# Optimization experiments

Hardware: AMD Instinct MI355X
Metric: run time of the kernel (lower is better)

Reference implementation:

```python
import jax, jax.numpy as jnp
import numpy as np

WS = (2, 7, 7)  # window size (T, H, W)
NUM_HEADS = 8


def _relative_position_index():
    t, h, w = WS
    coords = np.stack(np.meshgrid(np.arange(t), np.arange(h), np.arange(w), indexing='ij'))  # (3,t,h,w)
    flat = coords.reshape(3, -1)  # (3, N)
    rel = flat[:, :, None] - flat[:, None, :]  # (3, N, N)
    rel = rel.transpose(1, 2, 0).astype(np.int32)  # (N, N, 3)
    rel[..., 0] += t - 1
    rel[..., 1] += h - 1
    rel[..., 2] += w - 1
    rel[..., 0] *= (2 * h - 1) * (2 * w - 1)
    rel[..., 1] *= 2 * w - 1
    return rel.sum(-1)  # (N, N)


def setup_inputs() -> dict:
    key = jax.random.key(0)
    ks = jax.random.split(key, 7)
    B_, N, C = 2048, 98, 256
    nW = 512
    table_size = (2 * WS[0] - 1) * (2 * WS[1] - 1) * (2 * WS[2] - 1)  # 507
    return {
        'x': jax.random.normal(ks[0], (B_, N, C), jnp.float32),
        'mask': jax.random.normal(ks[1], (nW, N, N), jnp.float32),
        'qkv_w': jax.random.normal(ks[2], (3 * C, C), jnp.float32) * 0.02,
        'qkv_b': jax.random.normal(ks[3], (3 * C,), jnp.float32) * 0.02,
        'proj_w': jax.random.normal(ks[4], (C, C), jnp.float32) * 0.02,
        'proj_b': jax.random.normal(ks[5], (C,), jnp.float32) * 0.02,
        'bias_table': jax.random.normal(ks[6], (table_size, NUM_HEADS), jnp.float32) * 0.02,
        'rel_index': jnp.asarray(_relative_position_index()),
    }


def reference(x, mask, qkv_w, qkv_b, proj_w, proj_b, bias_table, rel_index):
    B_, N, C = x.shape
    H = NUM_HEADS
    hd = C // H
    scale = hd ** -0.5
    # QKV projection -> (3, B_, H, N, hd)
    qkv = (x @ qkv_w.T + qkv_b).reshape(B_, N, 3, H, hd).transpose(2, 0, 3, 1, 4)
    q, k, v = qkv[0], qkv[1], qkv[2]
    attn = jnp.einsum('bhnd,bhmd->bhnm', q * scale, k)  # (B_, H, N, N)
    # gathered relative-position bias -> (H, N, N)
    bias = bias_table[rel_index.reshape(-1)].reshape(N, N, H).transpose(2, 0, 1)
    attn = attn + bias[None]
    nW = mask.shape[0]
    attn = attn.reshape(B_ // nW, nW, H, N, N) + mask[None, :, None]
    attn = jax.nn.softmax(attn.reshape(B_, H, N, N), axis=-1)
    out = jnp.einsum('bhnm,bhmd->bhnd', attn, v)  # (B_, H, N, hd)
    out = out.transpose(0, 2, 1, 3).reshape(B_, N, C)
    return out @ proj_w.T + proj_b
```

## Files before the change

kernel.cpp:

```cpp
#include <hip/hip_runtime.h>
#include <hip/hip_bf16.h>

typedef __attribute__((ext_vector_type(8))) short short8;
typedef __attribute__((ext_vector_type(4))) float f32x4;

__device__ __forceinline__ unsigned short f2bf(float f) {
    __hip_bfloat16 h = __float2bfloat16(f);
    union { __hip_bfloat16 h; unsigned short u; } c; c.h = h; return c.u;
}

typedef __attribute__((address_space(1))) const unsigned int gas_u32;
typedef __attribute__((address_space(3))) unsigned int las_u32;

__device__ __forceinline__ void gload_lds16(const unsigned short* g, unsigned short* l) {
    __builtin_amdgcn_global_load_lds((gas_u32*)g, (las_u32*)l, 16, 0, 0);
}

__global__ void cvt_bf16_kernel(const float* __restrict__ src,
                                unsigned short* __restrict__ dst, long n8) {
    long stride = (long)gridDim.x * 256;
    for (long t = (long)blockIdx.x * 256 + threadIdx.x; t < n8; t += stride) {
        long i = t * 8;
        float4 f0 = *reinterpret_cast<const float4*>(src + i);
        float4 f1 = *reinterpret_cast<const float4*>(src + i + 4);
        uint4 u;
        u.x = ((unsigned)f2bf(f0.y) << 16) | f2bf(f0.x);
        u.y = ((unsigned)f2bf(f0.w) << 16) | f2bf(f0.z);
        u.z = ((unsigned)f2bf(f1.y) << 16) | f2bf(f1.x);
        u.w = ((unsigned)f2bf(f1.w) << 16) | f2bf(f1.z);
        *reinterpret_cast<uint4*>(dst + i) = u;
    }
}

__global__ void mask_pad_kernel(const float* __restrict__ mask,
                                float* __restrict__ mask_pad) {
    int idx = blockIdx.x * 256 + threadIdx.x;
    if (idx >= 512 * 12544) return;
    int w = idx / 12544, rem = idx - w * 12544;
    int n = rem / 112, m = rem - n * 112;
    float v;
    if (m >= 98) v = -1e30f;
    else if (n >= 98) v = 0.f;
    else v = mask[w * 9604 + n * 98 + m];
    mask_pad[idx] = v;
}

__global__ void bias_pad_kernel(const float* __restrict__ bias_table,
                                const int* __restrict__ rel_index,
                                float* __restrict__ bias_pad) {
    int idx = blockIdx.x * 256 + threadIdx.x;
    if (idx >= 8 * 12544) return;
    int h = idx / 12544, rem = idx - h * 12544;
    int n = rem / 112, m = rem - n * 112;
    float v = (n < 98 && m < 98) ? bias_table[rel_index[n * 98 + m] * 8 + h] : 0.f;
    bias_pad[idx] = v;
}

__global__ __launch_bounds__(256, 4)
void gemm_qkv_kernel(const unsigned short* __restrict__ Xb,
                     const unsigned short* __restrict__ Wb,
                     const float* __restrict__ bias,
                     unsigned short* __restrict__ qws,
                     unsigned short* __restrict__ kws,
                     unsigned short* __restrict__ vws) {
    __shared__ unsigned short sh[17408];
    unsigned short* As = sh;
    unsigned short* Bs = sh + 8192;
    const int tid = threadIdx.x;
    const int wave = tid >> 6, lane = tid & 63;
    const int q4 = lane >> 4, l16 = lane & 15;
    const int wr = wave >> 1, wc = wave & 1;

    const int nwg = gridDim.x * gridDim.y;
    const int bid = blockIdx.y * gridDim.x + blockIdx.x;
    const int swz = (bid & 7) * (nwg >> 3) + (bid >> 3);
    const int bx = swz % gridDim.x;
    const int by = swz / gridDim.x;

    const long m0 = (long)by * 128;
    const int n0 = bx * 128;

    const int srow = lane >> 3;
    const int scol = (lane & 7) << 3;

    f32x4 acc[4][4];
#pragma unroll
    for (int i = 0; i < 4; ++i)
#pragma unroll
        for (int j = 0; j < 4; ++j) acc[i][j] = (f32x4){0.f, 0.f, 0.f, 0.f};

    for (int ks = 0; ks < 256; ks += 64) {
#pragma unroll
        for (int i = 0; i < 4; ++i) {
            int c = wave * 4 + i;
            gload_lds16(Xb + (m0 + c * 8 + srow) * 256 + ks + scol, &As[c * 512]);
            gload_lds16(Wb + (long)(n0 + c * 8 + srow) * 256 + ks + scol, &Bs[c * 512]);
        }
        __syncthreads();
#pragma unroll
        for (int s = 0; s < 2; ++s) {
            short8 a[4], b[4];
#pragma unroll
            for (int i = 0; i < 4; ++i)
                a[i] = *reinterpret_cast<const short8*>(&As[(wr * 64 + i * 16 + l16) * 64 + s * 32 + q4 * 8]);
#pragma unroll
            for (int j = 0; j < 4; ++j)
                b[j] = *reinterpret_cast<const short8*>(&Bs[(wc * 64 + j * 16 + l16) * 64 + s * 32 + q4 * 8]);
#pragma unroll
            for (int i = 0; i < 4; ++i)
#pragma unroll
                for (int j = 0; j < 4; ++j)
                    acc[i][j] = __builtin_amdgcn_mfma_f32_16x16x32_bf16(a[i], b[j], acc[i][j], 0, 0, 0);
        }
        __syncthreads();
    }

    const float scale = (n0 < 256) ? 0.17677669529663687f : 1.0f;
#pragma unroll
    for (int i = 0; i < 4; ++i) {
#pragma unroll
        for (int j = 0; j < 4; ++j) {
            int c = wc * 64 + j * 16 + l16;
            float bcol = bias[n0 + c];
#pragma unroll
            for (int r = 0; r < 4; ++r) {
                int row = wr * 64 + i * 16 + q4 * 4 + r;
                sh[row * 136 + c] = f2bf((acc[i][j][r] + bcol) * scale);
            }
        }
    }
    __syncthreads();

    const int whichb = n0 >> 8;
    unsigned short* dstm = (whichb == 0) ? qws : ((whichb == 1) ? kws : vws);
    const int cbase = n0 & 255;
#pragma unroll
    for (int it = 0; it < 8; ++it) {
        int id = it * 256 + tid;
        int m = id >> 4;
        int ch = id & 15;
        uint4 u = *reinterpret_cast<const uint4*>(&sh[m * 136 + ch * 8]);
        long row = m0 + m;
        int b_ = (int)(row / 98);
        int n_ = (int)(row - (long)b_ * 98);
        int c = cbase + ch * 8;
        int h = c >> 5, d0 = c & 31;
        *reinterpret_cast<uint4*>(dstm + (((long)(b_ * 8 + h) * 98 + n_) * 32 + d0)) = u;
    }
}

__global__ __launch_bounds__(448, 7)
void attn_kernel(const unsigned short* __restrict__ q,
                 const unsigned short* __restrict__ k,
                 const unsigned short* __restrict__ v,
                 const float* __restrict__ mask_pad,
                 const float* __restrict__ bias_pad,
                 unsigned short* __restrict__ attn_out) {
    __shared__ unsigned short Qs[112 * 40];
    __shared__ unsigned short Ks[112 * 40];
    __shared__ unsigned short Vt[32 * 136];

    const int tid = threadIdx.x;
    const int wave = tid >> 6, lane = tid & 63;
    const int q4 = lane >> 4, l16 = lane & 15;

    const int d0_ = blockIdx.x;
    const int xcd = d0_ & 7, jj = d0_ >> 3;
    const int w = xcd * 64 + (jj >> 5);
    const int sub = jj & 31;
    const int b = (sub >> 3) * 512 + w;
    const int h = sub & 7;
    const int bh = b * 8 + h;
    const long base = (long)bh * 98 * 32;

    {
        int n = tid >> 2, dg = (tid & 3) * 8;
        uint4 vq = make_uint4(0, 0, 0, 0), vk = make_uint4(0, 0, 0, 0);
        if (n < 98) {
            vq = *reinterpret_cast<const uint4*>(q + base + n * 32 + dg);
            vk = *reinterpret_cast<const uint4*>(k + base + n * 32 + dg);
        }
        *reinterpret_cast<uint4*>(&Qs[n * 40 + dg]) = vq;
        *reinterpret_cast<uint4*>(&Ks[n * 40 + dg]) = vk;
    }
    for (int i = tid; i < 32 * 30; i += 448) {
        int d = i / 30, nn = 98 + (i - d * 30);
        Vt[d * 136 + nn] = 0;
    }
    {
        int n = tid >> 2, d0 = (tid & 3) * 8;
        if (n < 98) {
            union { uint4 u; unsigned short e[8]; } cvt;
            cvt.u = *reinterpret_cast<const uint4*>(v + base + n * 32 + d0);
#pragma unroll
            for (int kk = 0; kk < 8; ++kk) Vt[(d0 + kk) * 136 + n] = cvt.e[kk];
        }
    }
    __syncthreads();

    const float* mp = mask_pad + (long)w * 12544;
    const float* bp = bias_pad + (long)h * 12544;
    const long obase = (long)b * 98 * 256 + h * 32;

    const int tr = wave;
    const int n = tr * 16 + l16;
    const float* mrow = mp + n * 112;
    const float* brow = bp + n * 112;
    short8 bq = *reinterpret_cast<const short8*>(&Qs[n * 40 + q4 * 8]);
    f32x4 pv[7];
#pragma unroll
    for (int i = 0; i < 7; ++i) {
        short8 ak = *reinterpret_cast<const short8*>(&Ks[(i * 16 + l16) * 40 + q4 * 8]);
        f32x4 d = (f32x4){0.f, 0.f, 0.f, 0.f};
        d = __builtin_amdgcn_mfma_f32_16x16x32_bf16(ak, bq, d, 0, 0, 0);
        int m0 = i * 16 + q4 * 4;
        float4 mk = *reinterpret_cast<const float4*>(mrow + m0);
        float4 bb = *reinterpret_cast<const float4*>(brow + m0);
        pv[i][0] = d[0] + mk.x + bb.x;
        pv[i][1] = d[1] + mk.y + bb.y;
        pv[i][2] = d[2] + mk.z + bb.z;
        pv[i][3] = d[3] + mk.w + bb.w;
    }
    float mx = -1e30f;
#pragma unroll
    for (int i = 0; i < 7; ++i)
#pragma unroll
        for (int r = 0; r < 4; ++r) mx = fmaxf(mx, pv[i][r]);
    mx = fmaxf(mx, __shfl_xor(mx, 16));
    mx = fmaxf(mx, __shfl_xor(mx, 32));
    float sm = 0.f;
#pragma unroll
    for (int i = 0; i < 7; ++i)
#pragma unroll
        for (int r = 0; r < 4; ++r) {
            float e = __expf(pv[i][r] - mx);
            pv[i][r] = e;
            sm += e;
        }
    sm += __shfl_xor(sm, 16);
    sm += __shfl_xor(sm, 32);
    float rinv = 1.f / sm;
    unsigned up[8][2];
#pragma unroll
    for (int i = 0; i < 7; ++i) {
        up[i][0] = ((unsigned)f2bf(pv[i][1] * rinv) << 16) | f2bf(pv[i][0] * rinv);
        up[i][1] = ((unsigned)f2bf(pv[i][3] * rinv) << 16) | f2bf(pv[i][2] * rinv);
    }
    up[7][0] = 0; up[7][1] = 0;
    f32x4 o0 = (f32x4){0.f, 0.f, 0.f, 0.f};
    f32x4 o1 = (f32x4){0.f, 0.f, 0.f, 0.f};
    const int srcA = ((q4 & 1) * 2) * 16 + l16;
    const int srcB = srcA + 16;
    const bool hi = (q4 >= 2);
#pragma unroll
    for (int kc = 0; kc < 4; ++kc) {
        int ie = 2 * kc, io = 2 * kc + 1;
        unsigned a0e = __shfl(up[ie][0], srcA), a0o = __shfl(up[io][0], srcA);
        unsigned a1e = __shfl(up[ie][1], srcA), a1o = __shfl(up[io][1], srcA);
        unsigned b0e = __shfl(up[ie][0], srcB), b0o = __shfl(up[io][0], srcB);
        unsigned b1e = __shfl(up[ie][1], srcB), b1o = __shfl(up[io][1], srcB);
        union { uint4 u; short8 s; } cvt;
        cvt.u.x = hi ? a0o : a0e;
        cvt.u.y = hi ? a1o : a1e;
        cvt.u.z = hi ? b0o : b0e;
        cvt.u.w = hi ? b1o : b1e;
        short8 bv0 = *reinterpret_cast<const short8*>(&Vt[l16 * 136 + kc * 32 + q4 * 8]);
        short8 bv1 = *reinterpret_cast<const short8*>(&Vt[(16 + l16) * 136 + kc * 32 + q4 * 8]);
        o0 = __builtin_amdgcn_mfma_f32_16x16x32_bf16(cvt.s, bv0, o0, 0, 0, 0);
        o1 = __builtin_amdgcn_mfma_f32_16x16x32_bf16(cvt.s, bv1, o1, 0, 0, 0);
    }
#pragma unroll
    for (int r = 0; r < 4; ++r) {
        int nn = tr * 16 + q4 * 4 + r;
        if (nn < 98) {
            attn_out[obase + nn * 256 + l16] = f2bf(o0[r]);
            attn_out[obase + nn * 256 + 16 + l16] = f2bf(o1[r]);
        }
    }
}

__global__ __launch_bounds__(256, 4)
void gemm_proj_kernel(const unsigned short* __restrict__ Abf,
                      const unsigned short* __restrict__ Wb,
                      const float* __restrict__ bias,
                      float* __restrict__ out) {
    __shared__ unsigned short As[128 * 64];
    __shared__ unsigned short Bs[128 * 64];
    const int tid = threadIdx.x;
    const int wave = tid >> 6, lane = tid & 63;
    const int q4 = lane >> 4, l16 = lane & 15;
    const int wr = wave >> 1, wc = wave & 1;

    const int nwg = gridDim.x * gridDim.y;
    const int bid = blockIdx.y * gridDim.x + blockIdx.x;
    const int swz = (bid & 7) * (nwg >> 3) + (bid >> 3);
    const int bx = swz % gridDim.x;
    const int by = swz / gridDim.x;

    const long m0 = (long)by * 128;
    const int n0 = bx * 128;

    const int srow = lane >> 3;
    const int scol = (lane & 7) << 3;

    f32x4 acc[4][4];
#pragma unroll
    for (int i = 0; i < 4; ++i)
#pragma unroll
        for (int j = 0; j < 4; ++j) acc[i][j] = (f32x4){0.f, 0.f, 0.f, 0.f};

    for (int ks = 0; ks < 256; ks += 64) {
#pragma unroll
        for (int i = 0; i < 4; ++i) {
            int c = wave * 4 + i;
            gload_lds16(Abf + (m0 + c * 8 + srow) * 256 + ks + scol, &As[c * 512]);
            gload_lds16(Wb + (long)(n0 + c * 8 + srow) * 256 + ks + scol, &Bs[c * 512]);
        }
        __syncthreads();
#pragma unroll
        for (int s = 0; s < 2; ++s) {
            short8 a[4], b[4];
#pragma unroll
            for (int i = 0; i < 4; ++i)
                a[i] = *reinterpret_cast<const short8*>(&As[(wr * 64 + i * 16 + l16) * 64 + s * 32 + q4 * 8]);
#pragma unroll
            for (int j = 0; j < 4; ++j)
                b[j] = *reinterpret_cast<const short8*>(&Bs[(wc * 64 + j * 16 + l16) * 64 + s * 32 + q4 * 8]);
#pragma unroll
            for (int i = 0; i < 4; ++i)
#pragma unroll
                for (int j = 0; j < 4; ++j)
                    acc[i][j] = __builtin_amdgcn_mfma_f32_16x16x32_bf16(a[i], b[j], acc[i][j], 0, 0, 0);
        }
        __syncthreads();
    }
#pragma unroll
    for (int i = 0; i < 4; ++i) {
#pragma unroll
        for (int r = 0; r < 4; ++r) {
            long row = m0 + wr * 64 + i * 16 + q4 * 4 + r;
#pragma unroll
            for (int j = 0; j < 4; ++j) {
                int col = n0 + wc * 64 + j * 16 + l16;
                out[row * 256 + col] = acc[i][j][r] + bias[col];
            }
        }
    }
}

extern "C" void kernel_launch(void* const* d_in, const int* in_sizes, int n_in,
                              void* d_out, int out_size, void* d_ws, size_t ws_size,
                              hipStream_t stream) {
    (void)in_sizes; (void)n_in; (void)out_size; (void)ws_size;
    const float* x          = (const float*)d_in[0];
    const float* mask       = (const float*)d_in[1];
    const float* qkv_w      = (const float*)d_in[2];
    const float* qkv_b      = (const float*)d_in[3];
    const float* proj_w     = (const float*)d_in[4];
    const float* proj_b     = (const float*)d_in[5];
    const float* bias_table = (const float*)d_in[6];
    const int*   rel_index  = (const int*)d_in[7];
    float* out = (float*)d_out;

    const long QN = 51380224;
    unsigned short* qws  = (unsigned short*)d_ws;
    unsigned short* kws  = qws + QN;
    unsigned short* vws  = kws + QN;
    unsigned short* aow  = vws + QN;
    float* mask_padw = (float*)(aow + QN);
    float* bias_padw = mask_padw + 512 * 12544;
    unsigned short* wqkvb  = (unsigned short*)(bias_padw + 8 * 12544);
    unsigned short* wprojb = wqkvb + 768 * 256;
    unsigned short* xb = aow;

    mask_pad_kernel<<<dim3((512 * 12544 + 255) / 256), dim3(256), 0, stream>>>(
        mask, mask_padw);
    bias_pad_kernel<<<dim3((8 * 12544 + 255) / 256), dim3(256), 0, stream>>>(
        bias_table, rel_index, bias_padw);
    cvt_bf16_kernel<<<dim3(2048), dim3(256), 0, stream>>>(x, xb, 51380224L / 8);
    cvt_bf16_kernel<<<dim3(96), dim3(256), 0, stream>>>(qkv_w, wqkvb, 196608L / 8);
    cvt_bf16_kernel<<<dim3(32), dim3(256), 0, stream>>>(proj_w, wprojb, 65536L / 8);
    gemm_qkv_kernel<<<dim3(6, 1568), dim3(256), 0, stream>>>(
        xb, wqkvb, qkv_b, qws, kws, vws);
    attn_kernel<<<dim3(16384), dim3(448), 0, stream>>>(
        qws, kws, vws, mask_padw, bias_padw, aow);
    gemm_proj_kernel<<<dim3(2, 1568), dim3(256), 0, stream>>>(
        aow, wprojb, proj_b, out);
}
```

Measured before the change: 825.1 us.

## Read Q/K directly from global, stage P through LDS, fold log2e into softmax

The attention kernel now loads Q and K fragments straight from global memory instead of staging them in shared memory. The V load is issued early and its transpose into LDS is moved after the QK^T MFMAs to overlap latency. The softmax probabilities are written to a per-wave LDS buffer rather than reshuffled with many cross-lane shuffles. The log2e factor is folded into the Q scale, mask and bias so exp2f replaces __expf, and normalization is deferred to the output. This adds LDS usage (per-wave P buffers) and redundant global reads of K across waves, which may lower occupancy at 448 threads.

```diff
diff --git a/kernel.cpp b/kernel.cpp
--- a/kernel.cpp
+++ b/kernel.cpp
@@ -15,6 +15,8 @@
 __device__ __forceinline__ void gload_lds16(const unsigned short* g, unsigned short* l) {
     __builtin_amdgcn_global_load_lds((gas_u32*)g, (las_u32*)l, 16, 0, 0);
 }
+
+#define LOG2E 1.4426950408889634f
 
 __global__ void cvt_bf16_kernel(const float* __restrict__ src,
                                 unsigned short* __restrict__ dst, long n8) {
@@ -41,7 +43,7 @@
     float v;
     if (m >= 98) v = -1e30f;
     else if (n >= 98) v = 0.f;
-    else v = mask[w * 9604 + n * 98 + m];
+    else v = mask[w * 9604 + n * 98 + m] * LOG2E;
     mask_pad[idx] = v;
 }
 
@@ -52,7 +54,8 @@
     if (idx >= 8 * 12544) return;
     int h = idx / 12544, rem = idx - h * 12544;
     int n = rem / 112, m = rem - n * 112;
-    float v = (n < 98 && m < 98) ? bias_table[rel_index[n * 98 + m] * 8 + h] : 0.f;
+    float v = (n < 98 && m < 98)
+            ? bias_table[rel_index[n * 98 + m] * 8 + h] * LOG2E : 0.f;
     bias_pad[idx] = v;
 }
 
@@ -115,7 +118,7 @@
         __syncthreads();
     }
 
-    const float scale = (n0 < 256) ? 0.17677669529663687f : 1.0f;
+    const float scale = (n0 < 256) ? (0.17677669529663687f * LOG2E) : 1.0f;
 #pragma unroll
     for (int i = 0; i < 4; ++i) {
 #pragma unroll
@@ -156,9 +159,8 @@
                  const float* __restrict__ mask_pad,
                  const float* __restrict__ bias_pad,
                  unsigned short* __restrict__ attn_out) {
-    __shared__ unsigned short Qs[112 * 40];
-    __shared__ unsigned short Ks[112 * 40];
     __shared__ unsigned short Vt[32 * 136];
+    __shared__ unsigned short Pl[7 * 16 * 136];
 
     const int tid = threadIdx.x;
     const int wave = tid >> 6, lane = tid & 63;
@@ -173,44 +175,25 @@
     const int bh = b * 8 + h;
     const long base = (long)bh * 98 * 32;
 
-    {
-        int n = tid >> 2, dg = (tid & 3) * 8;
-        uint4 vq = make_uint4(0, 0, 0, 0), vk = make_uint4(0, 0, 0, 0);
-        if (n < 98) {
-            vq = *reinterpret_cast<const uint4*>(q + base + n * 32 + dg);
-            vk = *reinterpret_cast<const uint4*>(k + base + n * 32 + dg);
-        }
-        *reinterpret_cast<uint4*>(&Qs[n * 40 + dg]) = vq;
-        *reinterpret_cast<uint4*>(&Ks[n * 40 + dg]) = vk;
-    }
-    for (int i = tid; i < 32 * 30; i += 448) {
-        int d = i / 30, nn = 98 + (i - d * 30);
-        Vt[d * 136 + nn] = 0;
-    }
-    {
-        int n = tid >> 2, d0 = (tid & 3) * 8;
-        if (n < 98) {
-            union { uint4 u; unsigned short e[8]; } cvt;
-            cvt.u = *reinterpret_cast<const uint4*>(v + base + n * 32 + d0);
-#pragma unroll
-            for (int kk = 0; kk < 8; ++kk) Vt[(d0 + kk) * 136 + n] = cvt.e[kk];
-        }
-    }
-    __syncthreads();
-
-    const float* mp = mask_pad + (long)w * 12544;
-    const float* bp = bias_pad + (long)h * 12544;
-    const long obase = (long)b * 98 * 256 + h * 32;
+    const int vn = tid >> 2, vd0 = (tid & 3) * 8;
+    uint4 vval = make_uint4(0, 0, 0, 0);
+    if (vn < 98) vval = *reinterpret_cast<const uint4*>(v + base + vn * 32 + vd0);
 
     const int tr = wave;
     const int n = tr * 16 + l16;
-    const float* mrow = mp + n * 112;
-    const float* brow = bp + n * 112;
-    short8 bq = *reinterpret_cast<const short8*>(&Qs[n * 40 + q4 * 8]);
+    const int nq = n < 98 ? n : 97;
+
+    short8 bq = *reinterpret_cast<const short8*>(q + base + nq * 32 + q4 * 8);
+
+    const float* mrow = mask_pad + (long)w * 12544 + n * 112;
+    const float* brow = bias_pad + (long)h * 12544 + n * 112;
+
     f32x4 pv[7];
 #pragma unroll
     for (int i = 0; i < 7; ++i) {
-        short8 ak = *reinterpret_cast<const short8*>(&Ks[(i * 16 + l16) * 40 + q4 * 8]);
+        int kr = i * 16 + l16;
+        if (i == 6) kr = kr < 98 ? kr : 97;
+        short8 ak = *reinterpret_cast<const short8*>(k + base + kr * 32 + q4 * 8);
         f32x4 d = (f32x4){0.f, 0.f, 0.f, 0.f};
         d = __builtin_amdgcn_mfma_f32_16x16x32_bf16(ak, bq, d, 0, 0, 0);
         int m0 = i * 16 + q4 * 4;
@@ -221,6 +204,17 @@
         pv[i][2] = d[2] + mk.z + bb.z;
         pv[i][3] = d[3] + mk.w + bb.w;
     }
+
+    for (int idx = tid; idx < 32 * 30; idx += 448) {
+        int dd = idx / 30, nn = 98 + (idx - dd * 30);
+        Vt[dd * 136 + nn] = 0;
+    }
+    if (vn < 98) {
+        union { uint4 u; unsigned short e[8]; } cv; cv.u = vval;
+#pragma unroll
+        for (int kk = 0; kk < 8; ++kk) Vt[(vd0 + kk) * 136 + vn] = cv.e[kk];
+    }
+
     float mx = -1e30f;
 #pragma unroll
     for (int i = 0; i < 7; ++i)
@@ -233,48 +227,45 @@
     for (int i = 0; i < 7; ++i)
 #pragma unroll
         for (int r = 0; r < 4; ++r) {
-            float e = __expf(pv[i][r] - mx);
+            float e = exp2f(pv[i][r] - mx);
             pv[i][r] = e;
             sm += e;
         }
     sm += __shfl_xor(sm, 16);
     sm += __shfl_xor(sm, 32);
     float rinv = 1.f / sm;
-    unsigned up[8][2];
-#pragma unroll
-    for (int i = 0; i < 7; ++i) {
-        up[i][0] = ((unsigned)f2bf(pv[i][1] * rinv) << 16) | f2bf(pv[i][0] * rinv);
-        up[i][1] = ((unsigned)f2bf(pv[i][3] * rinv) << 16) | f2bf(pv[i][2] * rinv);
-    }
-    up[7][0] = 0; up[7][1] = 0;
+
+    unsigned short* Pw = Pl + wave * 2176;
+#pragma unroll
+    for (int i = 0; i < 8; ++i) {
+        unsigned lo = 0, hi = 0;
+        if (i < 7) {
+            lo = ((unsigned)f2bf(pv[i][1]) << 16) | f2bf(pv[i][0]);
+            hi = ((unsigned)f2bf(pv[i][3]) << 16) | f2bf(pv[i][2]);
+        }
+        *reinterpret_cast<uint2*>(&Pw[l16 * 136 + i * 16 + q4 * 4]) = make_uint2(lo, hi);
+    }
+    __syncthreads();
+
     f32x4 o0 = (f32x4){0.f, 0.f, 0.f, 0.f};
     f32x4 o1 = (f32x4){0.f, 0.f, 0.f, 0.f};
-    const int srcA = ((q4 & 1) * 2) * 16 + l16;
-    const int srcB = srcA + 16;
-    const bool hi = (q4 >= 2);
 #pragma unroll
     for (int kc = 0; kc < 4; ++kc) {
-        int ie = 2 * kc, io = 2 * kc + 1;
-        unsigned a0e = __shfl(up[ie][0], srcA), a0o = __shfl(up[io][0], srcA);
-        unsigned a1e = __shfl(up[ie][1], srcA), a1o = __shfl(up[io][1], srcA);
-        unsigned b0e = __shfl(up[ie][0], srcB), b0o = __shfl(up[io][0], srcB);
-        unsigned b1e = __shfl(up[ie][1], srcB), b1o = __shfl(up[io][1], srcB);
-        union { uint4 u; short8 s; } cvt;
-        cvt.u.x = hi ? a0o : a0e;
-        cvt.u.y = hi ? a1o : a1e;
-        cvt.u.z = hi ? b0o : b0e;
-        cvt.u.w = hi ? b1o : b1e;
+        short8 ap  = *reinterpret_cast<const short8*>(&Pw[l16 * 136 + kc * 32 + q4 * 8]);
         short8 bv0 = *reinterpret_cast<const short8*>(&Vt[l16 * 136 + kc * 32 + q4 * 8]);
         short8 bv1 = *reinterpret_cast<const short8*>(&Vt[(16 + l16) * 136 + kc * 32 + q4 * 8]);
-        o0 = __builtin_amdgcn_mfma_f32_16x16x32_bf16(cvt.s, bv0, o0, 0, 0, 0);
-        o1 = __builtin_amdgcn_mfma_f32_16x16x32_bf16(cvt.s, bv1, o1, 0, 0, 0);
-    }
+        o0 = __builtin_amdgcn_mfma_f32_16x16x32_bf16(ap, bv0, o0, 0, 0, 0);
+        o1 = __builtin_amdgcn_mfma_f32_16x16x32_bf16(ap, bv1, o1, 0, 0, 0);
+    }
+
+    const long obase = (long)b * 98 * 256 + h * 32;
 #pragma unroll
     for (int r = 0; r < 4; ++r) {
+        float rv = __shfl(rinv, q4 * 4 + r);
         int nn = tr * 16 + q4 * 4 + r;
         if (nn < 98) {
-            attn_out[obase + nn * 256 + l16] = f2bf(o0[r]);
-            attn_out[obase + nn * 256 + 16 + l16] = f2bf(o1[r]);
+            attn_out[obase + nn * 256 + l16] = f2bf(o0[r] * rv);
+            attn_out[obase + nn * 256 + 16 + l16] = f2bf(o1[r] * rv);
         }
     }
 }
```

New measurement: 1.205 ms. 1.46x slower.
